# Performance work log

Measured on AMD Instinct MI355X. Metric: run time of the kernel, lower is better.

The kernel has to match this reference:

```python
import jax, jax.numpy as jnp
import numpy as np

N_EMBD = 1024
N_HEAD = 16
B, T = 4, 2048

def setup_inputs() -> dict:
    key = jax.random.key(0)
    k1, k2, k3 = jax.random.split(key, 3)
    scale = 0.02
    return {
        "x": jax.random.normal(k1, (B, T, N_EMBD), dtype=jnp.float32),
        "W_qkv": jax.random.normal(k2, (N_EMBD, 3 * N_EMBD), dtype=jnp.float32) * scale,
        "b_qkv": jnp.zeros((3 * N_EMBD,), dtype=jnp.float32),
        "W_proj": jax.random.normal(k3, (N_EMBD, N_EMBD), dtype=jnp.float32) * scale,
        "b_proj": jnp.zeros((N_EMBD,), dtype=jnp.float32),
    }

def reference(x, W_qkv, b_qkv, W_proj, b_proj):
    Bb, Tt, C = x.shape
    hs = C // N_HEAD  # head_size
    qkv = x @ W_qkv + b_qkv                      # [B,T,3C]
    q, k, v = jnp.split(qkv, 3, axis=-1)
    # [B,T,C] -> [B,H,T,hs]
    def to_heads(t):
        return t.reshape(Bb, Tt, N_HEAD, hs).transpose(0, 2, 1, 3)
    q, k, v = to_heads(q), to_heads(k), to_heads(v)
    scores = jnp.einsum('bhqd,bhkd->bhqk', q, k) * (1.0 / np.sqrt(hs))
    causal = jnp.tril(jnp.ones((Tt, Tt), dtype=bool))
    scores = jnp.where(causal, scores, -jnp.inf)
    weights = jax.nn.softmax(scores, axis=-1)    # dropout=0.0 -> identity
    out = jnp.einsum('bhqk,bhkd->bhqd', weights, v)
    out = out.transpose(0, 2, 1, 3).reshape(Bb, Tt, C)
    return out @ W_proj + b_proj
```

## Files before the change

kernel.cpp:

```cpp
#include <hip/hip_runtime.h>
#include <cstdint>

typedef _Float16 f16;
typedef _Float16 f16x4 __attribute__((ext_vector_type(4)));
typedef _Float16 f16x8 __attribute__((ext_vector_type(8)));
typedef float f32x4 __attribute__((ext_vector_type(4)));

constexpr int NB = 4, NT = 2048, NC = 1024, NH = 16, HS = 64;
constexpr int Mtot = NB * NT;
constexpr int BM = 128, BN = 128;

__device__ __forceinline__ void gll16(const f16* g, f16* l) {
  __builtin_amdgcn_global_load_lds(
      (const __attribute__((address_space(1))) unsigned int*)(uintptr_t)g,
      (__attribute__((address_space(3))) unsigned int*)(uintptr_t)l, 16, 0, 0);
}

__global__ __launch_bounds__(256) void convert_x(
    const float* __restrict__ X, f16* __restrict__ Xh)
{
  const size_t i = ((size_t)blockIdx.x * 256 + threadIdx.x) * 8;
  float4 a = *reinterpret_cast<const float4*>(X + i);
  float4 b = *reinterpret_cast<const float4*>(X + i + 4);
  f16x8 o;
  o[0] = (f16)a.x; o[1] = (f16)a.y; o[2] = (f16)a.z; o[3] = (f16)a.w;
  o[4] = (f16)b.x; o[5] = (f16)b.y; o[6] = (f16)b.z; o[7] = (f16)b.w;
  *reinterpret_cast<f16x8*>(Xh + i) = o;
}

__global__ __launch_bounds__(256) void transpose_w(
    const float* __restrict__ Wq, const float* __restrict__ Wp,
    f16* __restrict__ Wqt, f16* __restrict__ Wpt)
{
  __shared__ __align__(16) f16 Ts[64 * 72];
  const int bx = blockIdx.x;
  const float* src; f16* dst; int Ndim, n0;
  if (bx < 48) { src = Wq; dst = Wqt; Ndim = 3 * NC; n0 = bx * 64; }
  else         { src = Wp; dst = Wpt; Ndim = NC;     n0 = (bx - 48) * 64; }
  const int k0 = blockIdx.y * 64;
  const int t = threadIdx.x;
  const int kl = t >> 2, nb = (t & 3) * 16;
#pragma unroll
  for (int i = 0; i < 4; ++i) {
    float4 vv = *reinterpret_cast<const float4*>(
        src + (size_t)(k0 + kl) * Ndim + n0 + nb + 4 * i);
    f16x4 h; h[0] = (f16)vv.x; h[1] = (f16)vv.y; h[2] = (f16)vv.z; h[3] = (f16)vv.w;
    *reinterpret_cast<f16x4*>(&Ts[kl * 72 + nb + 4 * i]) = h;
  }
  __syncthreads();
  const int nl = t >> 2, kb = (t & 3) * 16;
#pragma unroll
  for (int i = 0; i < 2; ++i) {
    f16x8 o;
#pragma unroll
    for (int j = 0; j < 8; ++j) o[j] = Ts[(kb + 8 * i + j) * 72 + nl];
    *reinterpret_cast<f16x8*>(dst + (size_t)(n0 + nl) * NC + k0 + kb + 8 * i) = o;
  }
}

template <int MODE>
__global__ __launch_bounds__(256) void gemm_f16(
    const f16* __restrict__ A, const f16* __restrict__ Bt,
    const float* __restrict__ bias,
    f16* __restrict__ Qh, f16* __restrict__ Kh, f16* __restrict__ Vh,
    float* __restrict__ Out, int ntiles)
{
  __shared__ __align__(16) f16 As[BM * 64];
  __shared__ __align__(16) f16 Bs[BN * 64];
  const int tid = threadIdx.x;
  const int flat = blockIdx.x;
  const int cpx = gridDim.x >> 3;
  const int v = (flat & 7) * cpx + (flat >> 3);
  const int m0 = (v / ntiles) * BM;
  const int n0 = (v % ntiles) * BN;
  const int w = tid >> 6, l = tid & 63;
  const int wr = w >> 1, wc = w & 1;
  const int lr = l & 15, hi = l >> 4;

  f32x4 acc[4][4];
#pragma unroll
  for (int i = 0; i < 4; ++i)
#pragma unroll
    for (int j = 0; j < 4; ++j) acc[i][j] = (f32x4){0.f, 0.f, 0.f, 0.f};

  const int lrow = l >> 3;
  const int lsrc = ((l & 7) ^ lrow) * 8;

  for (int k0 = 0; k0 < NC; k0 += 64) {
    __syncthreads();
#pragma unroll
    for (int i = 0; i < 4; ++i) {
      const int rr = 32 * w + 8 * i;
      gll16(A  + (size_t)(m0 + rr + lrow) * NC + k0 + lsrc, &As[rr * 64]);
      gll16(Bt + (size_t)(n0 + rr + lrow) * NC + k0 + lsrc, &Bs[rr * 64]);
    }
    __syncthreads();
#pragma unroll
    for (int kk = 0; kk < 2; ++kk) {
      f16x8 a[4], b[4];
#pragma unroll
      for (int mi = 0; mi < 4; ++mi) {
        int row = wr * 64 + mi * 16 + lr;
        int idx = (row * 64 + kk * 32 + hi * 8) ^ ((row & 7) << 3);
        a[mi] = *reinterpret_cast<const f16x8*>(&As[idx]);
      }
#pragma unroll
      for (int ni = 0; ni < 4; ++ni) {
        int row = wc * 64 + ni * 16 + lr;
        int idx = (row * 64 + kk * 32 + hi * 8) ^ ((row & 7) << 3);
        b[ni] = *reinterpret_cast<const f16x8*>(&Bs[idx]);
      }
#pragma unroll
      for (int mi = 0; mi < 4; ++mi)
#pragma unroll
        for (int ni = 0; ni < 4; ++ni)
          acc[mi][ni] = __builtin_amdgcn_mfma_f32_16x16x32_f16(
              a[mi], b[ni], acc[mi][ni], 0, 0, 0);
    }
  }

  if (MODE == 0) {
#pragma unroll
    for (int ni = 0; ni < 4; ++ni) {
      int colg = n0 + wc * 64 + ni * 16 + lr;
      int which = colg >> 10;
      int c = colg & (NC - 1);
      int h = c >> 6, d = c & 63;
      f16* dst = (which == 0) ? Qh : ((which == 1) ? Kh : Vh);
      float bv = bias[colg];
#pragma unroll
      for (int mi = 0; mi < 4; ++mi) {
#pragma unroll
        for (int r = 0; r < 4; ++r) {
          int rowg = m0 + wr * 64 + mi * 16 + hi * 4 + r;
          int b = rowg >> 11, t = rowg & (NT - 1);
          dst[(((size_t)(b * NH + h) * NT) + t) * HS + d] =
              (f16)(acc[mi][ni][r] + bv);
        }
      }
    }
  } else {
#pragma unroll
    for (int ni = 0; ni < 4; ++ni) {
      int colg = n0 + wc * 64 + ni * 16 + lr;
      float bv = bias[colg];
#pragma unroll
      for (int mi = 0; mi < 4; ++mi) {
#pragma unroll
        for (int r = 0; r < 4; ++r) {
          int rowg = m0 + wr * 64 + mi * 16 + hi * 4 + r;
          Out[(size_t)rowg * NC + colg] = acc[mi][ni][r] + bv;
        }
      }
    }
  }
}

__global__ __launch_bounds__(256, 2) void flash_attn(
    const f16* __restrict__ Qh, const f16* __restrict__ Kh,
    const f16* __restrict__ Vh, f16* __restrict__ att)
{
  __shared__ __align__(16) f16 Ks[2][64 * 64];
  __shared__ __align__(16) f16 Vt[2][64 * 64];
  __shared__ __align__(16) f16 Ps[4][32 * 64];

  const int tid = threadIdx.x;
  const int w = tid >> 6, l = tid & 63;
  const int lr = l & 15, g = l >> 4;

  const int flat = blockIdx.x;
  const int v = (flat & 7) * 64 + (flat >> 3);
  const int pairi = v & 7;
  const int bh = v >> 3;

  const f16* Qb = Qh + (size_t)bh * NT * HS;
  const f16* Kb = Kh + (size_t)bh * NT * HS;
  const f16* Vb = Vh + (size_t)bh * NT * HS;
  const int ob = bh >> 4, oh = bh & (NH - 1);

  const int srow = tid >> 2;
  const int scol = (tid & 3) * 16;

  f16x8 kpre[2], vpre[2];
#pragma unroll
  for (int ii = 0; ii < 2; ++ii) {
    kpre[ii] = *reinterpret_cast<const f16x8*>(Kb + (size_t)srow * HS + scol + 8 * ii);
    vpre[ii] = *reinterpret_cast<const f16x8*>(Vb + (size_t)srow * HS + scol + 8 * ii);
  }

  for (int seg = 0; seg < 2; ++seg) {
    const int qt = (seg == 0) ? pairi : 15 - pairi;
    const int qbase = qt * 128 + w * 32;
    const int jtmax = 2 * qt + 1;

    f16x8 qB[2][2];
#pragma unroll
    for (int mt = 0; mt < 2; ++mt)
#pragma unroll
      for (int ds = 0; ds < 2; ++ds) {
        f16x8 t = *reinterpret_cast<const f16x8*>(
            Qb + (size_t)(qbase + 16 * mt + lr) * HS + 32 * ds + 8 * g);
#pragma unroll
        for (int j = 0; j < 8; ++j) t[j] = t[j] * (f16)0.18033688f;
        qB[mt][ds] = t;
      }

    f32x4 Ot[2][4];
    float m_run[2], l_run[2];
#pragma unroll
    for (int mt = 0; mt < 2; ++mt) {
#pragma unroll
      for (int dt = 0; dt < 4; ++dt) Ot[mt][dt] = (f32x4){0.f, 0.f, 0.f, 0.f};
      m_run[mt] = -INFINITY; l_run[mt] = 0.f;
    }

    for (int jt = 0; jt <= jtmax; ++jt) {
      const int cur = jt & 1;
#pragma unroll
      for (int ii = 0; ii < 2; ++ii) {
        int c0 = scol + 8 * ii;
        *reinterpret_cast<f16x8*>(&Ks[cur][srow * 64 + (c0 ^ ((srow & 7) << 3))]) = kpre[ii];
#pragma unroll
        for (int j = 0; j < 8; ++j) {
          int d = c0 + j;
          int s = (d + (d >> 3)) & 7;
          Vt[cur][d * 64 + (srow ^ (s << 3))] = vpre[ii][j];
        }
      }
      const bool more = (jt < jtmax) || (seg == 0);
      if (more) {
        const int nj = (jt < jtmax) ? jt + 1 : 0;
#pragma unroll
        for (int ii = 0; ii < 2; ++ii) {
          kpre[ii] = *reinterpret_cast<const f16x8*>(
              Kb + (size_t)(nj * 64 + srow) * HS + scol + 8 * ii);
          vpre[ii] = *reinterpret_cast<const f16x8*>(
              Vb + (size_t)(nj * 64 + srow) * HS + scol + 8 * ii);
        }
      }
      __syncthreads();

      if (jt * 64 > qbase + 31) continue;

      const bool needMask = (jt * 64 + 63) > qbase;

      f16x8 aK[4][2];
#pragma unroll
      for (int kt2 = 0; kt2 < 4; ++kt2) {
        int row = 16 * kt2 + lr;
#pragma unroll
        for (int ds = 0; ds < 2; ++ds)
          aK[kt2][ds] = *reinterpret_cast<const f16x8*>(
              &Ks[cur][row * 64 + ((32 * ds + 8 * g) ^ ((row & 7) << 3))]);
      }

#pragma unroll
      for (int mt = 0; mt < 2; ++mt) {
        f32x4 St[4];
#pragma unroll
        for (int kt2 = 0; kt2 < 4; ++kt2) St[kt2] = (f32x4){0.f, 0.f, 0.f, 0.f};
        __builtin_amdgcn_s_setprio(1);
#pragma unroll
        for (int kt2 = 0; kt2 < 4; ++kt2)
#pragma unroll
          for (int ds = 0; ds < 2; ++ds)
            St[kt2] = __builtin_amdgcn_mfma_f32_16x16x32_f16(
                aK[kt2][ds], qB[mt][ds], St[kt2], 0, 0, 0);
        __builtin_amdgcn_s_setprio(0);

        const int qg = qbase + 16 * mt + lr;
        if (needMask) {
#pragma unroll
          for (int kt2 = 0; kt2 < 4; ++kt2)
#pragma unroll
            for (int r = 0; r < 4; ++r)
              if ((jt * 64 + 16 * kt2 + 4 * g + r) > qg) St[kt2][r] = -INFINITY;
        }
        float pm = -INFINITY;
#pragma unroll
        for (int kt2 = 0; kt2 < 4; ++kt2)
#pragma unroll
          for (int r = 0; r < 4; ++r) pm = fmaxf(pm, St[kt2][r]);
        pm = fmaxf(pm, __shfl_xor(pm, 16));
        pm = fmaxf(pm, __shfl_xor(pm, 32));
        const float mo = m_run[mt];
        const float mn = fmaxf(mo, pm);
        const float al = exp2f(mo - mn);
        m_run[mt] = mn;
        float ts = 0.f;
        const int q = 16 * mt + lr;
#pragma unroll
        for (int kt2 = 0; kt2 < 4; ++kt2) {
          float p0 = exp2f(St[kt2][0] - mn);
          float p1 = exp2f(St[kt2][1] - mn);
          float p2 = exp2f(St[kt2][2] - mn);
          float p3 = exp2f(St[kt2][3] - mn);
          ts += (p0 + p1) + (p2 + p3);
          f16x4 pk; pk[0] = (f16)p0; pk[1] = (f16)p1; pk[2] = (f16)p2; pk[3] = (f16)p3;
          *reinterpret_cast<f16x4*>(
              &Ps[w][q * 64 + ((16 * kt2 + 4 * g) ^ ((q & 7) << 3))]) = pk;
        }
        ts += __shfl_xor(ts, 16);
        ts += __shfl_xor(ts, 32);
        l_run[mt] = l_run[mt] * al + ts;
#pragma unroll
        for (int dt = 0; dt < 4; ++dt)
#pragma unroll
          for (int r = 0; r < 4; ++r) Ot[mt][dt][r] *= al;
      }

      __builtin_amdgcn_s_setprio(1);
#pragma unroll
      for (int kt = 0; kt < 2; ++kt) {
        f16x8 pB[2];
#pragma unroll
        for (int mt = 0; mt < 2; ++mt) {
          int q = 16 * mt + lr;
          pB[mt] = *reinterpret_cast<const f16x8*>(
              &Ps[w][q * 64 + ((32 * kt + 8 * g) ^ ((q & 7) << 3))]);
        }
#pragma unroll
        for (int dt = 0; dt < 4; ++dt) {
          int d = 16 * dt + lr;
          int s = (d + (d >> 3)) & 7;
          f16x8 vA = *reinterpret_cast<const f16x8*>(
              &Vt[cur][d * 64 + ((32 * kt + 8 * g) ^ (s << 3))]);
#pragma unroll
          for (int mt = 0; mt < 2; ++mt)
            Ot[mt][dt] = __builtin_amdgcn_mfma_f32_16x16x32_f16(
                vA, pB[mt], Ot[mt][dt], 0, 0, 0);
        }
      }
      __builtin_amdgcn_s_setprio(0);
    }

#pragma unroll
    for (int mt = 0; mt < 2; ++mt) {
      float inv = 1.f / l_run[mt];
      int q = 16 * mt + lr;
#pragma unroll
      for (int dt = 0; dt < 4; ++dt) {
        f16x4 ok;
#pragma unroll
        for (int r = 0; r < 4; ++r) ok[r] = (f16)(Ot[mt][dt][r] * inv);
        *reinterpret_cast<f16x4*>(
            &Ps[w][q * 64 + ((16 * dt + 4 * g) ^ ((q & 7) << 3))]) = ok;
      }
    }
    const int orow = l >> 1;
    const int ocol = (l & 1) * 32;
#pragma unroll
    for (int i = 0; i < 4; ++i) {
      f16x8 ov = *reinterpret_cast<const f16x8*>(
          &Ps[w][orow * 64 + ((ocol + i * 8) ^ ((orow & 7) << 3))]);
      *reinterpret_cast<f16x8*>(
          &att[((size_t)(ob * NT + qbase + orow)) * NC + oh * HS + ocol + i * 8]) = ov;
    }
  }
}

extern "C" void kernel_launch(void* const* d_in, const int* in_sizes, int n_in,
                              void* d_out, int out_size, void* d_ws, size_t ws_size,
                              hipStream_t stream)
{
  (void)in_sizes; (void)n_in; (void)out_size; (void)ws_size;
  const float* x     = (const float*)d_in[0];
  const float* Wqkv  = (const float*)d_in[1];
  const float* bqkv  = (const float*)d_in[2];
  const float* Wproj = (const float*)d_in[3];
  const float* bproj = (const float*)d_in[4];
  float* out = (float*)d_out;

  const size_t HE = (size_t)NB * NH * NT * HS;
  f16* Qh  = (f16*)d_ws;
  f16* Kh  = Qh + HE;
  f16* Vh  = Kh + HE;
  f16* XA  = Vh + HE;
  f16* Wqt = XA + HE;
  f16* Wpt = Wqt + (size_t)3 * NC * NC;

  convert_x<<<dim3(Mtot * NC / (256 * 8)), 256, 0, stream>>>(x, XA);
  transpose_w<<<dim3(64, 16), 256, 0, stream>>>(Wqkv, Wproj, Wqt, Wpt);
  gemm_f16<0><<<dim3(64 * 24), 256, 0, stream>>>(XA, Wqt, bqkv, Qh, Kh, Vh, nullptr, 24);
  flash_attn<<<dim3(512), 256, 0, stream>>>(Qh, Kh, Vh, XA);
  gemm_f16<1><<<dim3(64 * 8), 256, 0, stream>>>(XA, Wpt, bproj, nullptr, nullptr, nullptr, out, 8);
}
```

Measured before the change: 191.5 us.

## Keep softmax probabilities in registers and skip rescaling with lazy max threshold

Removes the per-warp LDS staging buffer for the probability tile. The V^T tile in shared memory is stored with a permuted key index so that the MFMA accumulator layout of the score tile can be fed directly as the B operand of the PV MFMA. It also adds a lazy online-softmax rescale that only updates the running max and rescales the output when the new max exceeds the old one by more than a threshold, saving exp and multiply work. Output staging now reuses the K buffer, which requires extra block barriers. The threshold lets probabilities exceed 1, giving some fp16 range risk.

```diff
diff --git a/kernel.cpp b/kernel.cpp
--- a/kernel.cpp
+++ b/kernel.cpp
@@ -162,7 +162,6 @@
 {
   __shared__ __align__(16) f16 Ks[2][64 * 64];
   __shared__ __align__(16) f16 Vt[2][64 * 64];
-  __shared__ __align__(16) f16 Ps[4][32 * 64];
 
   const int tid = threadIdx.x;
   const int w = tid >> 6, l = tid & 63;
@@ -180,6 +179,8 @@
 
   const int srow = tid >> 2;
   const int scol = (tid & 3) * 16;
+  const int ksl = ((srow >> 5) & 1) * 32 + ((srow >> 2) & 3) * 8 +
+                  ((srow >> 4) & 1) * 4 + (srow & 3);
 
   f16x8 kpre[2], vpre[2];
 #pragma unroll
@@ -224,7 +225,7 @@
         for (int j = 0; j < 8; ++j) {
           int d = c0 + j;
           int s = (d + (d >> 3)) & 7;
-          Vt[cur][d * 64 + (srow ^ (s << 3))] = vpre[ii][j];
+          Vt[cur][d * 64 + (ksl ^ (s << 3))] = vpre[ii][j];
         }
       }
       const bool more = (jt < jtmax) || (seg == 0);
@@ -254,6 +255,8 @@
               &Ks[cur][row * 64 + ((32 * ds + 8 * g) ^ ((row & 7) << 3))]);
       }
 
+      f16x8 pB[2][2];
+
 #pragma unroll
       for (int mt = 0; mt < 2; ++mt) {
         f32x4 St[4];
@@ -283,42 +286,36 @@
           for (int r = 0; r < 4; ++r) pm = fmaxf(pm, St[kt2][r]);
         pm = fmaxf(pm, __shfl_xor(pm, 16));
         pm = fmaxf(pm, __shfl_xor(pm, 32));
-        const float mo = m_run[mt];
-        const float mn = fmaxf(mo, pm);
-        const float al = exp2f(mo - mn);
-        m_run[mt] = mn;
+        float mo = m_run[mt];
+        if (!__all(pm <= mo + 8.0f)) {
+          float mn = fmaxf(mo, pm);
+          float al = exp2f(mo - mn);
+          l_run[mt] *= al;
+#pragma unroll
+          for (int dt = 0; dt < 4; ++dt)
+#pragma unroll
+            for (int r = 0; r < 4; ++r) Ot[mt][dt][r] *= al;
+          m_run[mt] = mn;
+          mo = mn;
+        }
         float ts = 0.f;
-        const int q = 16 * mt + lr;
 #pragma unroll
         for (int kt2 = 0; kt2 < 4; ++kt2) {
-          float p0 = exp2f(St[kt2][0] - mn);
-          float p1 = exp2f(St[kt2][1] - mn);
-          float p2 = exp2f(St[kt2][2] - mn);
-          float p3 = exp2f(St[kt2][3] - mn);
-          ts += (p0 + p1) + (p2 + p3);
-          f16x4 pk; pk[0] = (f16)p0; pk[1] = (f16)p1; pk[2] = (f16)p2; pk[3] = (f16)p3;
-          *reinterpret_cast<f16x4*>(
-              &Ps[w][q * 64 + ((16 * kt2 + 4 * g) ^ ((q & 7) << 3))]) = pk;
+#pragma unroll
+          for (int r = 0; r < 4; ++r) {
+            float pp = exp2f(St[kt2][r] - mo);
+            ts += pp;
+            pB[mt][kt2 >> 1][(kt2 & 1) * 4 + r] = (f16)pp;
+          }
         }
         ts += __shfl_xor(ts, 16);
         ts += __shfl_xor(ts, 32);
-        l_run[mt] = l_run[mt] * al + ts;
-#pragma unroll
-        for (int dt = 0; dt < 4; ++dt)
-#pragma unroll
-          for (int r = 0; r < 4; ++r) Ot[mt][dt][r] *= al;
+        l_run[mt] += ts;
       }
 
       __builtin_amdgcn_s_setprio(1);
 #pragma unroll
-      for (int kt = 0; kt < 2; ++kt) {
-        f16x8 pB[2];
-#pragma unroll
-        for (int mt = 0; mt < 2; ++mt) {
-          int q = 16 * mt + lr;
-          pB[mt] = *reinterpret_cast<const f16x8*>(
-              &Ps[w][q * 64 + ((32 * kt + 8 * g) ^ ((q & 7) << 3))]);
-        }
+      for (int kt = 0; kt < 2; ++kt)
 #pragma unroll
         for (int dt = 0; dt < 4; ++dt) {
           int d = 16 * dt + lr;
@@ -328,12 +325,13 @@
 #pragma unroll
           for (int mt = 0; mt < 2; ++mt)
             Ot[mt][dt] = __builtin_amdgcn_mfma_f32_16x16x32_f16(
-                vA, pB[mt], Ot[mt][dt], 0, 0, 0);
-        }
-      }
+                vA, pB[mt][kt], Ot[mt][dt], 0, 0, 0);
+        }
       __builtin_amdgcn_s_setprio(0);
     }
 
+    __syncthreads();
+    f16* scr = &Ks[0][0] + w * 2048;
 #pragma unroll
     for (int mt = 0; mt < 2; ++mt) {
       float inv = 1.f / l_run[mt];
@@ -344,7 +342,7 @@
 #pragma unroll
         for (int r = 0; r < 4; ++r) ok[r] = (f16)(Ot[mt][dt][r] * inv);
         *reinterpret_cast<f16x4*>(
-            &Ps[w][q * 64 + ((16 * dt + 4 * g) ^ ((q & 7) << 3))]) = ok;
+            &scr[q * 64 + ((16 * dt + 4 * g) ^ ((q & 7) << 3))]) = ok;
       }
     }
     const int orow = l >> 1;
@@ -352,10 +350,11 @@
 #pragma unroll
     for (int i = 0; i < 4; ++i) {
       f16x8 ov = *reinterpret_cast<const f16x8*>(
-          &Ps[w][orow * 64 + ((ocol + i * 8) ^ ((orow & 7) << 3))]);
+          &scr[orow * 64 + ((ocol + i * 8) ^ ((orow & 7) << 3))]);
       *reinterpret_cast<f16x8*>(
           &att[((size_t)(ob * NT + qbase + orow)) * NC + oh * HS + ocol + i * 8]) = ov;
     }
+    __syncthreads();
   }
 }
 
```

New measurement: 188.8 us. About the same (-1.4%).
